# Performance work log

Measured on AMD Instinct MI355X. Metric: run time of the kernel, lower is better.

## Reference

```python
import jax, jax.numpy as jnp
import numpy as np

D_IN = 1024
D_OUT = 1024
CTX_LEN = 2048
BATCH = 4
SEQ = 2048


def setup_inputs() -> dict:
    key = jax.random.key(0)
    kx, kq, kk, kv = jax.random.split(key, 4)
    x = jax.random.normal(kx, (BATCH, SEQ, D_IN), dtype=jnp.float32)
    s = 1.0 / np.sqrt(D_IN)
    # torch nn.Linear weight is (d_out, d_in); store transposed for x @ W
    W_q = jax.random.uniform(kq, (D_IN, D_OUT), dtype=jnp.float32, minval=-s, maxval=s)
    W_k = jax.random.uniform(kk, (D_IN, D_OUT), dtype=jnp.float32, minval=-s, maxval=s)
    W_v = jax.random.uniform(kv, (D_IN, D_OUT), dtype=jnp.float32, minval=-s, maxval=s)
    return {"x": x, "W_q": W_q, "W_k": W_k, "W_v": W_v}


def reference(x, W_q, W_k, W_v):
    b, n, _ = x.shape
    d_out = W_q.shape[1]
    q = x @ W_q            # [b, n, d_out]
    k = x @ W_k
    v = x @ W_v
    scores = jnp.einsum('bqd,bkd->bqk', q, k)  # [b, n, n]
    causal = jnp.triu(jnp.ones((n, n), dtype=bool), k=1)
    scores = jnp.where(causal, -jnp.inf, scores)
    attn = jax.nn.softmax(scores / jnp.sqrt(jnp.float32(d_out)), axis=-1)
    # dropout p=0.0 -> identity
    return jnp.einsum('bqk,bkd->bqd', attn, v)
```

## Files before the change

kernel.cpp:

```cpp
#include <hip/hip_runtime.h>
#include <hip/hip_bf16.h>

#define BATCH 4
#define SEQ   2048
#define DIN   1024
#define DOUT  1024
#define N3    3072
#define MTOT  (BATCH*SEQ)

typedef __hip_bfloat16 bf16;
typedef __attribute__((ext_vector_type(8))) short bf16x8;
typedef __attribute__((ext_vector_type(4))) float f32x4;

#define MFMA(a,b,c) __builtin_amdgcn_mfma_f32_16x16x32_bf16(a,b,c,0,0,0)

union pack4 { bf16 h[4]; uint2 u2; };
union pack8 { bf16 h[8]; bf16x8 v; };

__device__ __forceinline__ void gl16(const bf16* g, bf16* l)
{
    __builtin_amdgcn_global_load_lds(
        (const __attribute__((address_space(1))) void*)g,
        (__attribute__((address_space(3))) void*)l, 16, 0, 0);
}


__global__ __launch_bounds__(256)
void k_cvt_x(const float* __restrict__ x, bf16* __restrict__ xb)
{
    long i = ((long)blockIdx.x * 256 + threadIdx.x) * 4;
    float4 v = *(const float4*)(x + i);
    pack4 o;
    o.h[0] = __float2bfloat16(v.x);
    o.h[1] = __float2bfloat16(v.y);
    o.h[2] = __float2bfloat16(v.z);
    o.h[3] = __float2bfloat16(v.w);
    *(uint2*)(xb + i) = o.u2;
}

__global__ __launch_bounds__(256)
void k_cvt_w(const float* __restrict__ Wq, const float* __restrict__ Wk,
             const float* __restrict__ Wv, bf16* __restrict__ Wt)
{
    __shared__ bf16 t[64][68];
    const int mat = blockIdx.z;
    const float* W = (mat == 0) ? Wq : ((mat == 1) ? Wk : Wv);
    const int k0 = blockIdx.y * 64, n0 = blockIdx.x * 64;
#pragma unroll
    for (int p = 0; p < 4; ++p) {
        int kr = p * 16 + (threadIdx.x >> 4);
        int c4 = (threadIdx.x & 15) * 4;
        float4 v = *(const float4*)&W[(long)(k0 + kr) * DOUT + n0 + c4];
        t[c4 + 0][kr] = __float2bfloat16(v.x);
        t[c4 + 1][kr] = __float2bfloat16(v.y);
        t[c4 + 2][kr] = __float2bfloat16(v.z);
        t[c4 + 3][kr] = __float2bfloat16(v.w);
    }
    __syncthreads();
    bf16* O = Wt + (long)mat * DIN * DOUT;
#pragma unroll
    for (int i = 0; i < 2; ++i) {
        int l = threadIdx.x + i * 256;
        int n = l >> 3, c8 = (l & 7) * 8;
        pack8 o;
#pragma unroll
        for (int j = 0; j < 8; ++j) o.h[j] = t[n][c8 + j];
        *(bf16x8*)&O[(long)(n0 + n) * DIN + k0 + c8] = o.v;
    }
}


__device__ __forceinline__ void gemm_core(
    const bf16* __restrict__ Ab, long lda,
    const bf16* __restrict__ Bb, long ldb,
    int nk, bf16* __restrict__ As, bf16* __restrict__ Bs,
    f32x4 acc[4][4])
{
    const int tid  = threadIdx.x;
    const int lane = tid & 63;
    const int wave = tid >> 6;
    const int wm = (wave >> 1) * 64;
    const int wn = (wave & 1) * 64;
    const int r  = lane & 15;
    const int qd = lane >> 4;

    const int row0 = tid >> 3;
    const int c    = (tid & 7) ^ (row0 & 7);
    const long aoff = (long)row0 * lda + c * 8;
    const long boff = (long)row0 * ldb + c * 8;
    const long astep = 32 * lda, bstep = 32 * ldb;
    bf16* dA = &As[tid * 8];
    bf16* dB = &Bs[tid * 8];

    for (int kk = 0; kk < nk; ++kk) {
        const bf16* A = Ab + kk * 64 + aoff;
        const bf16* B = Bb + kk * 64 + boff;
#pragma unroll
        for (int i = 0; i < 4; ++i) {
            gl16(A + i * astep, dA + i * 2048);
            gl16(B + i * bstep, dB + i * 2048);
        }
        __syncthreads();
#pragma unroll
        for (int ks = 0; ks < 2; ++ks) {
            const int slot = ((ks * 4 + qd) ^ (r & 7)) * 8;
            bf16x8 af[4], bv[4];
#pragma unroll
            for (int mi = 0; mi < 4; ++mi)
                af[mi] = *(const bf16x8*)&As[(wm + mi * 16 + r) * 64 + slot];
#pragma unroll
            for (int ni = 0; ni < 4; ++ni)
                bv[ni] = *(const bf16x8*)&Bs[(wn + ni * 16 + r) * 64 + slot];
#pragma unroll
            for (int mi = 0; mi < 4; ++mi)
#pragma unroll
                for (int ni = 0; ni < 4; ++ni)
                    acc[mi][ni] = MFMA(af[mi], bv[ni], acc[mi][ni]);
        }
        __syncthreads();
    }
}


__global__ __launch_bounds__(256)
void k_gemm_qkv(const bf16* __restrict__ xb, const bf16* __restrict__ Wt,
                bf16* __restrict__ QKV)
{
    __shared__ __align__(16) bf16 As[128 * 64];
    __shared__ __align__(16) bf16 Bs[128 * 64];
    const int m0 = blockIdx.y * 128, n0 = blockIdx.x * 128;
    f32x4 acc[4][4] = {};
    gemm_core(xb + (long)m0 * DIN, DIN, Wt + (long)n0 * DIN, DIN, DIN / 64, As, Bs, acc);

    const int lane = threadIdx.x & 63, wave = threadIdx.x >> 6;
    const int wm = (wave >> 1) * 64, wn = (wave & 1) * 64;
    const int r = lane & 15, qd = lane >> 4;
#pragma unroll
    for (int mi = 0; mi < 4; ++mi)
#pragma unroll
        for (int ni = 0; ni < 4; ++ni)
#pragma unroll
            for (int j = 0; j < 4; ++j) {
                int row = m0 + wm + mi * 16 + qd * 4 + j;
                int col = n0 + wn + ni * 16 + r;
                QKV[(long)row * N3 + col] = __float2bfloat16(acc[mi][ni][j]);
            }
}


__global__ __launch_bounds__(256)
void k_transpose_v(const bf16* __restrict__ QKV, bf16* __restrict__ Vt)
{
    __shared__ __align__(16) bf16 t[64][80];
    const int b = blockIdx.z;
    const int s0 = blockIdx.x * 64, d0 = blockIdx.y * 64;
    const bf16* Vb = QKV + (long)b * SEQ * N3 + 2048;
#pragma unroll
    for (int i = 0; i < 2; ++i) {
        int l = threadIdx.x + i * 256;
        int sl = l >> 3, c8 = (l & 7) * 8;
        *(bf16x8*)&t[sl][c8] = *(const bf16x8*)&Vb[(long)(s0 + sl) * N3 + d0 + c8];
    }
    __syncthreads();
    bf16* Ob = Vt + (long)b * DOUT * SEQ;
#pragma unroll
    for (int i = 0; i < 2; ++i) {
        int l = threadIdx.x + i * 256;
        int dl = l >> 3, s8 = (l & 7) * 8;
        pack8 o;
#pragma unroll
        for (int j = 0; j < 8; ++j) o.h[j] = t[s8 + j][dl];
        *(bf16x8*)&Ob[(long)(d0 + dl) * SEQ + s0 + s8] = o.v;
    }
}


__global__ __launch_bounds__(256)
void k_gemm_scores(const bf16* __restrict__ QKV, float* __restrict__ S)
{
    const int b = blockIdx.z, qt = blockIdx.y, kt = blockIdx.x;
    if (kt > qt) return;
    __shared__ __align__(16) bf16 As[128 * 64];
    __shared__ __align__(16) bf16 Bs[128 * 64];
    const bf16* A  = QKV + (long)b * SEQ * N3;
    const bf16* Bt = A + 1024;
    f32x4 acc[4][4] = {};
    gemm_core(A + (long)qt * 128 * N3, N3, Bt + (long)kt * 128 * N3, N3,
              DIN / 64, As, Bs, acc);

    float* Sb = S + (long)b * SEQ * SEQ;
    const int lane = threadIdx.x & 63, wave = threadIdx.x >> 6;
    const int wm = (wave >> 1) * 64, wn = (wave & 1) * 64;
    const int r = lane & 15, qd = lane >> 4;
#pragma unroll
    for (int mi = 0; mi < 4; ++mi)
#pragma unroll
        for (int ni = 0; ni < 4; ++ni)
#pragma unroll
            for (int j = 0; j < 4; ++j) {
                int row = qt * 128 + wm + mi * 16 + qd * 4 + j;
                int col = kt * 128 + wn + ni * 16 + r;
                float v = acc[mi][ni][j] * 0.03125f;
                if (col > row) v = -1e30f;
                Sb[(long)row * SEQ + col] = v;
            }
}


__global__ __launch_bounds__(256)
void k_softmax(float* __restrict__ S)
{
    const int wave = threadIdx.x >> 6, lane = threadIdx.x & 63;
    const int rowIdx = blockIdx.x * 4 + wave;
    const int qrow = rowIdx & (SEQ - 1);
    const int lim = ((qrow >> 7) + 1) * 128;
    const int niter = (lim + 255) >> 8;
    float* Srow = S + (long)rowIdx * SEQ;

    float4 v[8];
    float m = -1e30f;
#pragma unroll
    for (int i = 0; i < 8; ++i) {
        if (i < niter) {
            int base = (i * 64 + lane) * 4;
            float4 t = ((const float4*)Srow)[i * 64 + lane];
            if (base >= lim) { t.x = -1e30f; t.y = -1e30f; t.z = -1e30f; t.w = -1e30f; }
            v[i] = t;
            m = fmaxf(m, fmaxf(fmaxf(t.x, t.y), fmaxf(t.z, t.w)));
        }
    }
#pragma unroll
    for (int d = 1; d < 64; d <<= 1) m = fmaxf(m, __shfl_xor(m, d, 64));
    float sum = 0.f;
#pragma unroll
    for (int i = 0; i < 8; ++i) {
        if (i < niter) {
            v[i].x = __expf(v[i].x - m);
            v[i].y = __expf(v[i].y - m);
            v[i].z = __expf(v[i].z - m);
            v[i].w = __expf(v[i].w - m);
            sum += (v[i].x + v[i].y) + (v[i].z + v[i].w);
        }
    }
#pragma unroll
    for (int d = 1; d < 64; d <<= 1) sum += __shfl_xor(sum, d, 64);
    const float inv = 1.0f / sum;

    bf16* P = (bf16*)Srow;
#pragma unroll
    for (int i = 0; i < 8; ++i) {
        if (i < niter) {
            pack4 o;
            o.h[0] = __float2bfloat16(v[i].x * inv);
            o.h[1] = __float2bfloat16(v[i].y * inv);
            o.h[2] = __float2bfloat16(v[i].z * inv);
            o.h[3] = __float2bfloat16(v[i].w * inv);
            *(uint2*)(P + (i * 64 + lane) * 4) = o.u2;
        }
    }
}


__global__ __launch_bounds__(256)
void k_gemm_pv(const float* __restrict__ Sf, const bf16* __restrict__ Vt,
               float* __restrict__ O)
{
    const int b = blockIdx.z, nt = blockIdx.x;
    const int qt = (SEQ / 128 - 1) - blockIdx.y;
    __shared__ __align__(16) bf16 As[128 * 64];
    __shared__ __align__(16) bf16 Bs[128 * 64];
    const bf16* A  = (const bf16*)(Sf + (long)b * SEQ * SEQ);
    const bf16* Bt = Vt + (long)b * DOUT * SEQ;
    const int nk = (qt + 1) * 2;
    f32x4 acc[4][4] = {};
    gemm_core(A + (long)qt * 128 * 4096, 4096, Bt + (long)nt * 128 * SEQ, SEQ,
              nk, As, Bs, acc);

    float* Ob = O + (long)b * SEQ * DOUT;
    const int lane = threadIdx.x & 63, wave = threadIdx.x >> 6;
    const int wm = (wave >> 1) * 64, wn = (wave & 1) * 64;
    const int r = lane & 15, qd = lane >> 4;
#pragma unroll
    for (int mi = 0; mi < 4; ++mi)
#pragma unroll
        for (int ni = 0; ni < 4; ++ni)
#pragma unroll
            for (int j = 0; j < 4; ++j) {
                int row = qt * 128 + wm + mi * 16 + qd * 4 + j;
                int col = nt * 128 + wn + ni * 16 + r;
                Ob[(long)row * DOUT + col] = acc[mi][ni][j];
            }
}


extern "C" void kernel_launch(void* const* d_in, const int* in_sizes, int n_in,
                              void* d_out, int out_size, void* d_ws, size_t ws_size,
                              hipStream_t stream)
{
    const float* x  = (const float*)d_in[0];
    const float* Wq = (const float*)d_in[1];
    const float* Wk = (const float*)d_in[2];
    const float* Wv = (const float*)d_in[3];
    float* out = (float*)d_out;

    char* ws = (char*)d_ws;
    bf16*  xb  = (bf16*)(ws);
    bf16*  Wt  = (bf16*)(ws + 16777216);
    bf16*  QKV = (bf16*)(ws + 23068672);
    bf16*  Vt  = (bf16*)(ws + 73400320);
    float* S   = (float*)(ws + 90177536);

    k_cvt_x<<<dim3(MTOT * DIN / (256 * 4)), 256, 0, stream>>>(x, xb);
    k_cvt_w<<<dim3(DOUT / 64, DIN / 64, 3), 256, 0, stream>>>(Wq, Wk, Wv, Wt);
    k_gemm_qkv<<<dim3(N3 / 128, MTOT / 128), 256, 0, stream>>>(xb, Wt, QKV);
    k_transpose_v<<<dim3(SEQ / 64, DOUT / 64, BATCH), 256, 0, stream>>>(QKV, Vt);
    k_gemm_scores<<<dim3(SEQ / 128, SEQ / 128, BATCH), 256, 0, stream>>>(QKV, S);
    k_softmax<<<dim3(MTOT / 4), 256, 0, stream>>>(S);
    k_gemm_pv<<<dim3(DOUT / 128, SEQ / 128, BATCH), 256, 0, stream>>>(S, Vt, out);
}
```

Baseline: 260.0 us.

## Fuse softmax into scores GEMM epilogue with deferred normalization via atomic row sums

Computes exp of the scaled scores directly in the QK^T GEMM epilogue and writes unnormalized bf16 probabilities. Row sums are accumulated with atomics into a small buffer. The PV GEMM divides its output by the row sum. This removes the separate softmax pass and the fp32 score-matrix traffic. It drops the max subtraction, which risks overflow for large scores, and adds atomics plus a memset.

```diff
diff --git a/kernel.cpp b/kernel.cpp
--- a/kernel.cpp
+++ b/kernel.cpp
@@ -176,7 +176,8 @@
 
 
 __global__ __launch_bounds__(256)
-void k_gemm_scores(const bf16* __restrict__ QKV, float* __restrict__ S)
+void k_gemm_scores(const bf16* __restrict__ QKV, bf16* __restrict__ P,
+                   float* __restrict__ rowSum)
 {
     const int b = blockIdx.z, qt = blockIdx.y, kt = blockIdx.x;
     if (kt > qt) return;
@@ -188,10 +189,18 @@
     gemm_core(A + (long)qt * 128 * N3, N3, Bt + (long)kt * 128 * N3, N3,
               DIN / 64, As, Bs, acc);
 
-    float* Sb = S + (long)b * SEQ * SEQ;
+    bf16* Pb = P + (long)b * SEQ * SEQ;
+    float* RS = rowSum + b * SEQ;
     const int lane = threadIdx.x & 63, wave = threadIdx.x >> 6;
     const int wm = (wave >> 1) * 64, wn = (wave & 1) * 64;
     const int r = lane & 15, qd = lane >> 4;
+
+    float rp[4][4];
+#pragma unroll
+    for (int mi = 0; mi < 4; ++mi)
+#pragma unroll
+        for (int j = 0; j < 4; ++j) rp[mi][j] = 0.f;
+
 #pragma unroll
     for (int mi = 0; mi < 4; ++mi)
 #pragma unroll
@@ -200,96 +209,60 @@
             for (int j = 0; j < 4; ++j) {
                 int row = qt * 128 + wm + mi * 16 + qd * 4 + j;
                 int col = kt * 128 + wn + ni * 16 + r;
-                float v = acc[mi][ni][j] * 0.03125f;
-                if (col > row) v = -1e30f;
-                Sb[(long)row * SEQ + col] = v;
-            }
-}
-
-
-__global__ __launch_bounds__(256)
-void k_softmax(float* __restrict__ S)
-{
-    const int wave = threadIdx.x >> 6, lane = threadIdx.x & 63;
-    const int rowIdx = blockIdx.x * 4 + wave;
-    const int qrow = rowIdx & (SEQ - 1);
-    const int lim = ((qrow >> 7) + 1) * 128;
-    const int niter = (lim + 255) >> 8;
-    float* Srow = S + (long)rowIdx * SEQ;
-
-    float4 v[8];
-    float m = -1e30f;
-#pragma unroll
-    for (int i = 0; i < 8; ++i) {
-        if (i < niter) {
-            int base = (i * 64 + lane) * 4;
-            float4 t = ((const float4*)Srow)[i * 64 + lane];
-            if (base >= lim) { t.x = -1e30f; t.y = -1e30f; t.z = -1e30f; t.w = -1e30f; }
-            v[i] = t;
-            m = fmaxf(m, fmaxf(fmaxf(t.x, t.y), fmaxf(t.z, t.w)));
-        }
-    }
-#pragma unroll
-    for (int d = 1; d < 64; d <<= 1) m = fmaxf(m, __shfl_xor(m, d, 64));
-    float sum = 0.f;
-#pragma unroll
-    for (int i = 0; i < 8; ++i) {
-        if (i < niter) {
-            v[i].x = __expf(v[i].x - m);
-            v[i].y = __expf(v[i].y - m);
-            v[i].z = __expf(v[i].z - m);
-            v[i].w = __expf(v[i].w - m);
-            sum += (v[i].x + v[i].y) + (v[i].z + v[i].w);
-        }
-    }
-#pragma unroll
-    for (int d = 1; d < 64; d <<= 1) sum += __shfl_xor(sum, d, 64);
-    const float inv = 1.0f / sum;
-
-    bf16* P = (bf16*)Srow;
-#pragma unroll
-    for (int i = 0; i < 8; ++i) {
-        if (i < niter) {
-            pack4 o;
-            o.h[0] = __float2bfloat16(v[i].x * inv);
-            o.h[1] = __float2bfloat16(v[i].y * inv);
-            o.h[2] = __float2bfloat16(v[i].z * inv);
-            o.h[3] = __float2bfloat16(v[i].w * inv);
-            *(uint2*)(P + (i * 64 + lane) * 4) = o.u2;
-        }
-    }
-}
-
-
-__global__ __launch_bounds__(256)
-void k_gemm_pv(const float* __restrict__ Sf, const bf16* __restrict__ Vt,
-               float* __restrict__ O)
+                float e = (col > row) ? 0.f : __expf(acc[mi][ni][j] * 0.03125f);
+                rp[mi][j] += e;
+                Pb[(long)row * SEQ + col] = __float2bfloat16(e);
+            }
+#pragma unroll
+    for (int d = 1; d < 16; d <<= 1)
+#pragma unroll
+        for (int mi = 0; mi < 4; ++mi)
+#pragma unroll
+            for (int j = 0; j < 4; ++j)
+                rp[mi][j] += __shfl_xor(rp[mi][j], d, 64);
+    if (r == 0) {
+#pragma unroll
+        for (int mi = 0; mi < 4; ++mi)
+#pragma unroll
+            for (int j = 0; j < 4; ++j) {
+                int row = qt * 128 + wm + mi * 16 + qd * 4 + j;
+                atomicAdd(&RS[row], rp[mi][j]);
+            }
+    }
+}
+
+
+__global__ __launch_bounds__(256)
+void k_gemm_pv(const bf16* __restrict__ P, const bf16* __restrict__ Vt,
+               const float* __restrict__ rowSum, float* __restrict__ O)
 {
     const int b = blockIdx.z, nt = blockIdx.x;
     const int qt = (SEQ / 128 - 1) - blockIdx.y;
     __shared__ __align__(16) bf16 As[128 * 64];
     __shared__ __align__(16) bf16 Bs[128 * 64];
-    const bf16* A  = (const bf16*)(Sf + (long)b * SEQ * SEQ);
+    const bf16* A  = P + (long)b * SEQ * SEQ + (long)qt * 128 * SEQ;
     const bf16* Bt = Vt + (long)b * DOUT * SEQ;
     const int nk = (qt + 1) * 2;
     f32x4 acc[4][4] = {};
-    gemm_core(A + (long)qt * 128 * 4096, 4096, Bt + (long)nt * 128 * SEQ, SEQ,
-              nk, As, Bs, acc);
+    gemm_core(A, SEQ, Bt + (long)nt * 128 * SEQ, SEQ, nk, As, Bs, acc);
 
     float* Ob = O + (long)b * SEQ * DOUT;
+    const float* RS = rowSum + b * SEQ;
     const int lane = threadIdx.x & 63, wave = threadIdx.x >> 6;
     const int wm = (wave >> 1) * 64, wn = (wave & 1) * 64;
     const int r = lane & 15, qd = lane >> 4;
 #pragma unroll
     for (int mi = 0; mi < 4; ++mi)
 #pragma unroll
-        for (int ni = 0; ni < 4; ++ni)
-#pragma unroll
-            for (int j = 0; j < 4; ++j) {
-                int row = qt * 128 + wm + mi * 16 + qd * 4 + j;
+        for (int j = 0; j < 4; ++j) {
+            int row = qt * 128 + wm + mi * 16 + qd * 4 + j;
+            float inv = 1.0f / RS[row];
+#pragma unroll
+            for (int ni = 0; ni < 4; ++ni) {
                 int col = nt * 128 + wn + ni * 16 + r;
-                Ob[(long)row * DOUT + col] = acc[mi][ni][j];
-            }
+                Ob[(long)row * DOUT + col] = acc[mi][ni][j] * inv;
+            }
+        }
 }
 
 
@@ -308,13 +281,14 @@
     bf16*  Wt  = (bf16*)(ws + 16777216);
     bf16*  QKV = (bf16*)(ws + 23068672);
     bf16*  Vt  = (bf16*)(ws + 73400320);
-    float* S   = (float*)(ws + 90177536);
-
+    bf16*  P   = (bf16*)(ws + 90177536);
+    float* RS  = (float*)(ws + 123731968);
+
+    hipMemsetAsync(RS, 0, BATCH * SEQ * sizeof(float), stream);
     k_cvt_x<<<dim3(MTOT * DIN / (256 * 4)), 256, 0, stream>>>(x, xb);
     k_cvt_w<<<dim3(DOUT / 64, DIN / 64, 3), 256, 0, stream>>>(Wq, Wk, Wv, Wt);
     k_gemm_qkv<<<dim3(N3 / 128, MTOT / 128), 256, 0, stream>>>(xb, Wt, QKV);
     k_transpose_v<<<dim3(SEQ / 64, DOUT / 64, BATCH), 256, 0, stream>>>(QKV, Vt);
-    k_gemm_scores<<<dim3(SEQ / 128, SEQ / 128, BATCH), 256, 0, stream>>>(QKV, S);
-    k_softmax<<<dim3(MTOT / 4), 256, 0, stream>>>(S);
-    k_gemm_pv<<<dim3(DOUT / 128, SEQ / 128, BATCH), 256, 0, stream>>>(S, Vt, out);
-}
+    k_gemm_scores<<<dim3(SEQ / 128, SEQ / 128, BATCH), 256, 0, stream>>>(QKV, P, RS);
+    k_gemm_pv<<<dim3(DOUT / 128, SEQ / 128, BATCH), 256, 0, stream>>>(P, Vt, RS, out);
+}
```

New measurement: 254.1 us. 2.3% less time.
